# Kernel optimization log

Hardware: AMD Instinct MI355X
Metric: run time of the kernel (lower is better)

Reference implementation:

```python
import jax, jax.numpy as jnp
import numpy as np
from jax import lax

COUNTER_TARGET = 40
CONV_THRESH = 0.01


def compute_ellipticity(images):
    """images: [B,H,W] -> (e1[B], e2[B]) via iterative adaptive-Gaussian moments."""
    B, H, W = images.shape
    y = jnp.arange(H, dtype=jnp.float32) - H / 2.0 + 0.5
    x = jnp.arange(W, dtype=jnp.float32) - W / 2.0 + 0.5
    Y, X = jnp.meshgrid(y, x, indexing='ij')  # [H,W]
    X = X[None]  # [1,H,W]
    Y = Y[None]
    total = jnp.sum(images, axis=(1, 2))
    image_area = jnp.float32(H * W)

    def cond_fn(c):
        i, ax, ay, axy, mux, muy, psxx, psyy, csxx, csyy, back, e1, e2 = c
        first = jnp.equal(i, 0)
        valid = jnp.logical_not(jnp.any(jnp.isnan(csxx))) & jnp.logical_not(jnp.any(jnp.isnan(csyy)))
        converged = (jnp.max(jnp.abs(csxx - psxx)) < CONV_THRESH) & (jnp.max(jnp.abs(csyy - psyy)) < CONV_THRESH)
        converged = converged & jnp.logical_not(first)
        return (i < COUNTER_TARGET) & valid & (first | jnp.logical_not(converged))

    def body_fn(c):
        i, ax, ay, axy, mux, muy, psxx, psyy, csxx, csyy, back, e1, e2 = c
        ax = jnp.clip(ax, 0.5, 20.0)
        ay = jnp.clip(ay, 0.5, 20.0)
        axy = jnp.clip(axy, -10.0, 10.0)
        Xc = X - mux[:, None, None]
        Yc = Y - muy[:, None, None]
        alpha_denom = jnp.maximum(ax * ay, 1e-8)
        alpha_ratio = jnp.clip(axy / alpha_denom, -0.95, 0.95)
        arb_const = jnp.maximum(2.0 * (1.0 - alpha_ratio ** 2), 1e-8)
        sqrt_term = jnp.maximum(1.0 - alpha_ratio ** 2, 1e-8)
        A = 1.0 / (2.0 * jnp.pi * alpha_denom * jnp.sqrt(sqrt_term))
        A = jnp.clip(A, 1e-10, 1e10)
        ax_sq = jnp.maximum(ax ** 2, 1e-8)
        ay_sq = jnp.maximum(ay ** 2, 1e-8)
        e1t = Xc ** 2 / (arb_const * ax_sq)[:, None, None]
        e2t = Yc ** 2 / (arb_const * ay_sq)[:, None, None]
        e3t = 2.0 * axy[:, None, None] * Xc * Yc / (arb_const * ax_sq * ay_sq)[:, None, None]
        exp_term = jnp.clip(e1t + e2t - e3t, 0.0, 30.0)
        k = A[:, None, None] * jnp.exp(-exp_term)
        k = jnp.where(jnp.isnan(k), 0.0, k)
        k = jnp.where(jnp.isinf(k), 0.0, k)
        img1 = images - back[:, None, None]
        ik = img1 * k
        t1 = jnp.sum(X * Y * ik, axis=(1, 2))
        t2 = jnp.sum(ik, axis=(1, 2))
        t3 = jnp.sum(X * ik, axis=(1, 2))
        t4 = jnp.sum(Y * ik, axis=(1, 2))
        t5 = jnp.sum(X * X * ik, axis=(1, 2))
        t6 = jnp.sum(Y * Y * ik, axis=(1, 2))
        t7 = jnp.sum(k * k, axis=(1, 2))
        t2s = jnp.maximum(jnp.abs(t2), 1e-6)
        t7s = jnp.maximum(t7, 1e-6)
        flux_calc = t2 / t7s
        new_back = jnp.clip((total - flux_calc) / image_area, -1.0, 1.0)
        new_mux = jnp.clip(t3 / t2s, -W / 2.0, W / 2.0)
        new_muy = jnp.clip(t4 / t2s, -H / 2.0, H / 2.0)
        sigxx = t5 / t2s - (t3 / t2s) ** 2
        sigyy = t6 / t2s - (t4 / t2s) ** 2
        sigxy = t1 / t2s - t3 * t4 / (t2s * t2s)
        sigxx = jnp.clip(sigxx, 0.25, 100.0)
        sigyy = jnp.clip(sigyy, 0.25, 100.0)
        sigxy = jnp.clip(sigxy, -50.0, 50.0)
        nax = jnp.sqrt(jnp.clip(sigxx * 2.0, 1.0, 400.0))
        nay = jnp.sqrt(jnp.clip(sigyy * 2.0, 1.0, 400.0))
        naxy = jnp.clip(2.0 * sigxy, -20.0, 20.0)
        denom = jnp.maximum(sigxx + sigyy, 1e-6)
        ne1 = jnp.clip((sigxx - sigyy) / denom, -0.95, 0.95)
        ne2 = jnp.clip(2.0 * sigxy / denom, -0.95, 0.95)
        ne1 = jnp.where(jnp.isnan(ne1), 0.0, ne1)
        ne2 = jnp.where(jnp.isnan(ne2), 0.0, ne2)
        nax = jnp.where(jnp.isnan(nax), 2.0, nax)
        nay = jnp.where(jnp.isnan(nay), 2.0, nay)
        naxy = jnp.where(jnp.isnan(naxy), 0.0, naxy)
        return (i + 1, nax, nay, naxy, new_mux, new_muy, csxx, csyy, sigxx, sigyy, new_back, ne1, ne2)

    def step(c, _):
        cont = cond_fn(c)
        nc = body_fn(c)
        c = jax.tree_util.tree_map(lambda a, b: jnp.where(cont, b, a), c, nc)
        return c, None

    init = (jnp.int32(0),
            jnp.full([B], 2.0), jnp.full([B], 2.0), jnp.zeros([B]),
            jnp.zeros([B]), jnp.zeros([B]),
            jnp.full([B], 4.0), jnp.full([B], 4.0),
            jnp.zeros([B]), jnp.zeros([B]),
            jnp.zeros([B]), jnp.zeros([B]), jnp.zeros([B]))
    final, _ = lax.scan(step, init, None, length=COUNTER_TARGET)
    e1, e2 = final[11], final[12]
    e1 = jnp.where(jnp.isnan(e1) | jnp.isinf(e1), 0.0, e1)
    e2 = jnp.where(jnp.isnan(e2) | jnp.isinf(e2), 0.0, e2)
    return e1, e2


def blur_with_kernel(image, kernel):
    """image [B,H,W,1], kernel [B,kH,kW,1] -> per-sample SAME conv (correlation)."""
    def single(img, ker):
        ker = ker / (jnp.sum(ker) + 1e-6)
        ker = ker[..., None]  # [kH,kW,1,1] HWIO
        out = lax.conv_general_dilated(img[None], ker, window_strides=(1, 1),
                                       padding='SAME',
                                       dimension_numbers=('NHWC', 'HWIO', 'NHWC'))
        return out[0]
    return jax.vmap(single)(image, kernel)


def setup_inputs() -> dict:
    key = jax.random.key(0)
    ks = jax.random.split(key, 5)
    B, H, W, kH = 512, 96, 96, 31
    return {
        'y_pred': jax.random.uniform(ks[0], (B, H, W, 1), dtype=jnp.float32),
        'y_true': jax.random.uniform(ks[1], (B, H, W, 1), dtype=jnp.float32),
        'blurred_img': jax.random.uniform(ks[2], (B, H, W, 2), dtype=jnp.float32),
        'kernel_img': jax.random.uniform(ks[3], (B, kH, kH, 1), dtype=jnp.float32),
        'weight_map': jax.random.uniform(ks[4], (B, H, W, 1), dtype=jnp.float32),
        'current_epoch': 3,
    }


def reference(y_pred, y_true, blurred_img, kernel_img, weight_map, current_epoch):
    weighted_mse = jnp.mean(jnp.square(y_pred - y_true) * weight_map)
    sharp_true = jnp.squeeze(y_true, axis=-1)
    sharp_pred = jnp.squeeze(y_pred, axis=-1)
    e1_t, e2_t = compute_ellipticity(sharp_true)
    e1_p, e2_p = compute_ellipticity(sharp_pred)
    ellip_diff = jnp.mean((e1_t - e1_p) ** 2 + (e2_t - e2_p) ** 2)
    ellip_loss = jnp.clip(ellip_diff, 0.0, 1.0)
    ellip_weight = 0.01 + 0.1 * jnp.float32(min(current_epoch, 4))
    original_blurred = blurred_img[:, :, :, 0:1]
    reblurred = blur_with_kernel(y_pred, kernel_img)
    reblur_loss = jnp.mean(jnp.square(reblurred - original_blurred) * weight_map)
    total_loss = 100.0 * weighted_mse + 100.0 * reblur_loss + ellip_weight * ellip_loss
    return total_loss
```

## Files before the change

kernel.cpp:

```cpp
#include <hip/hip_runtime.h>

#define HW 9216
#define NBATCH 512

__device__ __forceinline__ float clampf(float v, float lo, float hi){ return fminf(fmaxf(v, lo), hi); }

__device__ __forceinline__ float waveSum(float v){
#pragma unroll
  for (int o = 32; o; o >>= 1) v += __shfl_xor(v, o, 64);
  return v;
}

__global__ __launch_bounds__(256) void mse_kernel(const float4* __restrict__ yp,
                                                  const float4* __restrict__ yt,
                                                  const float4* __restrict__ wm,
                                                  float* __restrict__ partial){
  __shared__ float red[4];
  const int tid = threadIdx.x;
  int idx = blockIdx.x * 256 + tid;
  float s = 0.f;
#pragma unroll
  for (int u = 0; u < 9; ++u){
    float4 a = yp[idx], b = yt[idx], w = wm[idx];
    float dx = a.x-b.x, dy = a.y-b.y, dz = a.z-b.z, dw = a.w-b.w;
    s += dx*dx*w.x + dy*dy*w.y + dz*dz*w.z + dw*dw*w.w;
    idx += 131072;
  }
  s = waveSum(s);
  if ((tid & 63) == 0) red[tid >> 6] = s;
  __syncthreads();
  if (tid == 0) partial[blockIdx.x] = red[0]+red[1]+red[2]+red[3];
}

__global__ __launch_bounds__(256)
void ellip_kernel(const float* __restrict__ y_true,
                  const float* __restrict__ y_pred,
                  float2* __restrict__ ebuf){
  __shared__ float wred[7][4];
  __shared__ float tred[4];
  typedef __fp16 half2_t __attribute__((ext_vector_type(2)));
  const int tid  = threadIdx.x;
  const int wave = tid >> 6, lane = tid & 63;
  const int d = blockIdx.x >> 9;
  const int b = blockIdx.x & 511;
  const int tx = tid & 31, ty = tid >> 5;

  const float* src = (d ? y_pred : y_true) + (size_t)b * HW + ty * 96 + tx;

  unsigned px2[6][3];
  float tot = 0.f;
#pragma unroll
  for (int jj = 0; jj < 6; ++jj){
#pragma unroll
    for (int c = 0; c < 3; ++c){
      float ve = src[jj*1536 + c*32];
      float vo = src[jj*1536 + 768 + c*32];
      tot += ve + vo;
      half2_t pk = __builtin_amdgcn_cvt_pkrtz(ve, vo);
      unsigned u = __builtin_bit_cast(unsigned, pk);
      asm volatile("" : "+v"(u));
      px2[jj][c] = u;
    }
  }
  tot = waveSum(tot);
  if (lane == 0) tred[wave] = tot;
  __syncthreads();
  float total;
  { float4 t = *reinterpret_cast<const float4*>(&tred[0]); total = (t.x+t.y)+(t.z+t.w); }
  __syncthreads();

  const float Ya00 = (float)ty - 47.5f;
  float Xa[3];
#pragma unroll
  for (int c = 0; c < 3; ++c){ Xa[c] = (float)(tx + 32*c) - 47.5f; }

  float zx=4.f, zy=4.f, axy=0.f, mux=0.f, muy=0.f, back=0.f, e1=0.f, e2=0.f;
  const float LOG2E = 1.4426950408889634f;
  const float NQLO  = -43.280851226668906f;

  for (int it = 0; it < 40; ++it){
    float axyc = clampf(axy, -10.f, 10.f);
    float prod = zx*zy;
    float adn  = sqrtf(prod);
    float rca  = __builtin_amdgcn_rcpf(adn);
    float ar   = clampf(axyc*rca, -0.95f, 0.95f);
    float omr  = fmaf(-ar, ar, 1.f);
    float A    = 0.15915494309189535f * rca * __builtin_amdgcn_rsqf(omr);
    float invq = __builtin_amdgcn_rcpf(2.f*omr*prod);
    float a1 = -LOG2E*zy*invq;
    float a2 = -LOG2E*zx*invq;
    float a3 = (2.f*LOG2E)*axyc*invq;
    float cX2[3], cX3[3];
#pragma unroll
    for (int c = 0; c < 3; ++c){
      float Xc = Xa[c] - mux;
      cX2[c] = a1*Xc*Xc;
      cX3[c] = a3*Xc;
    }
    float S0[3] = {0.f,0.f,0.f}, SY[3] = {0.f,0.f,0.f};
    float tYY = 0.f, tkk = 0.f;
#pragma unroll
    for (int jj = 0; jj < 6; ++jj){
      float Yae = Ya00 + 16.f*jj;
      float Yao = Yae + 8.f;
      float Yce = Yae - muy, Yco = Yao - muy;
      float he = a2*Yce*Yce, ho = a2*Yco*Yco;
      float rse = 0.f, rso = 0.f;
#pragma unroll
      for (int c = 0; c < 3; ++c){
        half2_t pk = __builtin_bit_cast(half2_t, px2[jj][c]);
        float pe = (float)pk.x, po = (float)pk.y;
        {
          float nq = fmaf(cX3[c], Yce, he + cX2[c]);
          float e  = __builtin_amdgcn_exp2f(fminf(fmaxf(nq, NQLO), 0.f));
          float ik = (pe - back)*e;
          S0[c] += ik;  SY[c] = fmaf(Yae, ik, SY[c]);  tkk = fmaf(e, e, tkk);  rse += ik;
        }
        {
          float nq = fmaf(cX3[c], Yco, ho + cX2[c]);
          float e  = __builtin_amdgcn_exp2f(fminf(fmaxf(nq, NQLO), 0.f));
          float ik = (po - back)*e;
          S0[c] += ik;  SY[c] = fmaf(Yao, ik, SY[c]);  tkk = fmaf(e, e, tkk);  rso += ik;
        }
      }
      tYY = fmaf(Yae*Yae, rse, fmaf(Yao*Yao, rso, tYY));
    }
    float tik = S0[0]+S0[1]+S0[2];
    float tX  = fmaf(Xa[2],S0[2], fmaf(Xa[1],S0[1], Xa[0]*S0[0]));
    float tXX = fmaf(Xa[2]*Xa[2],S0[2], fmaf(Xa[1]*Xa[1],S0[1], (Xa[0]*Xa[0])*S0[0]));
    float tY  = SY[0]+SY[1]+SY[2];
    float tXY = fmaf(Xa[2],SY[2], fmaf(Xa[1],SY[1], Xa[0]*SY[0]));
    tXY=waveSum(tXY); tik=waveSum(tik); tX=waveSum(tX); tY=waveSum(tY);
    tXX=waveSum(tXX); tYY=waveSum(tYY); tkk=waveSum(tkk);
    if (lane == 0){
      wred[0][wave]=tXY; wred[1][wave]=tik; wred[2][wave]=tX; wred[3][wave]=tY;
      wred[4][wave]=tXX; wred[5][wave]=tYY; wred[6][wave]=tkk;
    }
    __syncthreads();
    float T[7];
#pragma unroll
    for (int k = 0; k < 7; ++k){
      float4 r = *reinterpret_cast<const float4*>(&wred[k][0]);
      T[k] = (r.x+r.y)+(r.z+r.w);
    }
    __syncthreads();
    float T1=T[0]*A, T2=T[1]*A, T3=T[2]*A, T4=T[3]*A, T5=T[4]*A, T6=T[5]*A, T7=T[6]*A*A;
    float t2s = fmaxf(fabsf(T2), 1e-6f);
    float rt2 = __builtin_amdgcn_rcpf(t2s);
    float flux = T2 * __builtin_amdgcn_rcpf(fmaxf(T7, 1e-6f));
    back = clampf((total - flux) * (1.f/9216.f), -1.f, 1.f);
    float r3 = T3*rt2, r4 = T4*rt2;
    mux = clampf(r3, -48.f, 48.f);
    muy = clampf(r4, -48.f, 48.f);
    float sxx = clampf(T5*rt2 - r3*r3, 0.25f, 100.f);
    float syy = clampf(T6*rt2 - r4*r4, 0.25f, 100.f);
    float sxy = clampf(T1*rt2 - T3*T4*rt2*rt2, -50.f, 50.f);
    zx = clampf(sxx*2.f, 1.f, 400.f);
    zy = clampf(syy*2.f, 1.f, 400.f);
    axy = clampf(2.f*sxy, -20.f, 20.f);
    float rden = __builtin_amdgcn_rcpf(sxx+syy);
    e1 = clampf((sxx-syy)*rden, -0.95f, 0.95f);
    e2 = clampf(2.f*sxy*rden, -0.95f, 0.95f);
  }
  if (tid == 0) ebuf[d*512 + b] = make_float2(e1, e2);
}

__global__ __launch_bounds__(384, 6) void conv_kernel(const float* __restrict__ y_pred,
                                                      const float* __restrict__ kimg,
                                                      const float* __restrict__ blurred,
                                                      const float* __restrict__ wmap,
                                                      float* __restrict__ partial){
  __shared__ float P[78*128];
  __shared__ float red[6];
  const int tid = threadIdx.x;
  const int bb = blockIdx.x, b = bb >> 1, h = bb & 1;
  const int R0 = h * 48;
  const int wave = tid >> 6, lane = tid & 63;

  const float* img = y_pred + (size_t)b * HW;
  for (int u = tid; u < 78*128; u += 384){
    int pr = u >> 7, pc = u & 127;
    int ir = R0 - 15 + pr, ic = pc - 16;
    float v = 0.f;
    if ((unsigned)ir < 96u && (unsigned)ic < 96u) v = img[ir*96 + ic];
    P[u] = v;
  }
  const float* kb = kimg + (size_t)b * 961;
  float ks = 0.f;
  for (int u = tid; u < 961; u += 384) ks += kb[u];
  ks = waveSum(ks);
  if (lane == 0) red[wave] = ks;
  __syncthreads();
  const float inv = __fdividef(1.f, (red[0]+red[1]+red[2]+red[3]+red[4]+red[5]) + 1e-6f);

  const int cs = tid % 24, rq = tid / 24;
  const int c = cs*4;
  const int rr0 = R0 + rq*3;
  float acc[3][4];
#pragma unroll
  for (int q = 0; q < 3; ++q){
#pragma unroll
    for (int j = 0; j < 4; ++j) acc[q][j] = 0.f;
  }

#pragma unroll 1
  for (int s = 0; s < 33; ++s){
    float w[36];
    const float4* prow = reinterpret_cast<const float4*>(&P[(rq*3 + s)*128 + c]);
#pragma unroll
    for (int m = 0; m < 9; ++m){
      float4 v = prow[m];
      w[4*m+0]=v.x; w[4*m+1]=v.y; w[4*m+2]=v.z; w[4*m+3]=v.w;
    }
#pragma unroll
    for (int q = 0; q < 3; ++q){
      const int dy = s - q;
      if (dy >= 0 && dy <= 30){
        const float* kr = kb + dy*31;
#pragma unroll
        for (int dx = 0; dx < 31; ++dx){
          const float kv = kr[dx];
          acc[q][0] = fmaf(kv, w[dx+1], acc[q][0]);
          acc[q][1] = fmaf(kv, w[dx+2], acc[q][1]);
          acc[q][2] = fmaf(kv, w[dx+3], acc[q][2]);
          acc[q][3] = fmaf(kv, w[dx+4], acc[q][3]);
        }
      }
    }
  }

  float lsum = 0.f;
#pragma unroll
  for (int q = 0; q < 3; ++q){
#pragma unroll
    for (int j = 0; j < 4; ++j){
      const int rr = rr0+q, cc = c+j;
      const size_t pix = (size_t)b*HW + rr*96 + cc;
      float ov = acc[q][j] * inv;
      float dd = ov - blurred[2*pix];
      lsum = fmaf(dd*dd, wmap[pix], lsum);
    }
  }
  lsum = waveSum(lsum);
  __syncthreads();
  if (lane == 0) red[wave] = lsum;
  __syncthreads();
  if (tid == 0) partial[bb] = red[0]+red[1]+red[2]+red[3]+red[4]+red[5];
}

__global__ __launch_bounds__(512) void final_kernel(const float* __restrict__ msep,
                                                    const float* __restrict__ convp,
                                                    const float2* __restrict__ ebuf,
                                                    const int* __restrict__ epoch,
                                                    float* __restrict__ out){
  __shared__ float red[3][8];
  const int tid = threadIdx.x, wave = tid >> 6, lane = tid & 63;
  float a = msep[tid];
  float bsum = convp[tid] + convp[512 + tid];
  float2 et = ebuf[tid], ep = ebuf[512 + tid];
  float dx = et.x - ep.x, dy = et.y - ep.y;
  float c = dx*dx + dy*dy;
  a = waveSum(a); bsum = waveSum(bsum); c = waveSum(c);
  if (lane == 0){ red[0][wave]=a; red[1][wave]=bsum; red[2][wave]=c; }
  __syncthreads();
  if (tid == 0){
    float sa=0, sb=0, sc=0;
#pragma unroll
    for (int w = 0; w < 8; ++w){ sa+=red[0][w]; sb+=red[1][w]; sc+=red[2][w]; }
    float mse   = sa / 4718592.f;
    float rebl  = sb / 4718592.f;
    float ediff = clampf(sc / 512.f, 0.f, 1.f);
    int e = *epoch; if (e > 4) e = 4;
    float ew = 0.01f + 0.1f * (float)e;
    out[0] = 100.f*mse + 100.f*rebl + ew*ediff;
  }
}

extern "C" void kernel_launch(void* const* d_in, const int* in_sizes, int n_in,
                              void* d_out, int out_size, void* d_ws, size_t ws_size,
                              hipStream_t stream){
  const float* y_pred  = (const float*)d_in[0];
  const float* y_true  = (const float*)d_in[1];
  const float* blurred = (const float*)d_in[2];
  const float* kimg    = (const float*)d_in[3];
  const float* wmap    = (const float*)d_in[4];
  const int*   epoch   = (const int*)d_in[5];
  float* out = (float*)d_out;
  float* ws  = (float*)d_ws;

  float*  msep  = ws;
  float*  convp = ws + 512;
  float2* ebufp = (float2*)(ws + 1536);

  mse_kernel<<<512, 256, 0, stream>>>((const float4*)y_pred, (const float4*)y_true,
                                      (const float4*)wmap, msep);

  ellip_kernel<<<1024, 256, 0, stream>>>(y_true, y_pred, ebufp);

  conv_kernel<<<1024, 384, 0, stream>>>(y_pred, kimg, blurred, wmap, convp);

  final_kernel<<<1, 512, 0, stream>>>(msep, convp, ebufp, epoch, out);
}
```

Baseline: 347.2 us.

## Fuse ellipticity and convolution kernels into one interleaved launch

```diff
diff --git a/kernel.cpp b/kernel.cpp
--- a/kernel.cpp
+++ b/kernel.cpp
@@ -32,220 +32,231 @@
   if (tid == 0) partial[blockIdx.x] = red[0]+red[1]+red[2]+red[3];
 }
 
-__global__ __launch_bounds__(256)
-void ellip_kernel(const float* __restrict__ y_true,
+__global__ __launch_bounds__(384, 6)
+void fused_kernel(const float* __restrict__ y_true,
                   const float* __restrict__ y_pred,
-                  float2* __restrict__ ebuf){
-  __shared__ float wred[7][4];
-  __shared__ float tred[4];
+                  const float* __restrict__ kimg,
+                  const float* __restrict__ blurred,
+                  const float* __restrict__ wmap,
+                  float2* __restrict__ ebuf,
+                  float* __restrict__ convp){
+  extern __shared__ float smem[];
   typedef __fp16 half2_t __attribute__((ext_vector_type(2)));
-  const int tid  = threadIdx.x;
+  const int tid = threadIdx.x;
+  const int bid = blockIdx.x;
+  const int id  = bid >> 1;
   const int wave = tid >> 6, lane = tid & 63;
-  const int d = blockIdx.x >> 9;
-  const int b = blockIdx.x & 511;
-  const int tx = tid & 31, ty = tid >> 5;
-
-  const float* src = (d ? y_pred : y_true) + (size_t)b * HW + ty * 96 + tx;
-
-  unsigned px2[6][3];
-  float tot = 0.f;
-#pragma unroll
-  for (int jj = 0; jj < 6; ++jj){
-#pragma unroll
-    for (int c = 0; c < 3; ++c){
-      float ve = src[jj*1536 + c*32];
-      float vo = src[jj*1536 + 768 + c*32];
-      tot += ve + vo;
-      half2_t pk = __builtin_amdgcn_cvt_pkrtz(ve, vo);
-      unsigned u = __builtin_bit_cast(unsigned, pk);
-      asm volatile("" : "+v"(u));
-      px2[jj][c] = u;
-    }
+
+  if ((bid & 1) == 0){
+    float (*wred)[4] = (float(*)[4])smem;
+    float* tred = smem + 28;
+    if (tid < 256){
+      const int d = id >> 9;
+      const int b = id & 511;
+      const int tx = tid & 31, ty = tid >> 5;
+
+      const float* src = (d ? y_pred : y_true) + (size_t)b * HW + ty * 96 + tx;
+
+      unsigned px2[6][3];
+      float tot = 0.f;
+#pragma unroll
+      for (int jj = 0; jj < 6; ++jj){
+#pragma unroll
+        for (int c = 0; c < 3; ++c){
+          float ve = src[jj*1536 + c*32];
+          float vo = src[jj*1536 + 768 + c*32];
+          tot += ve + vo;
+          half2_t pk = __builtin_amdgcn_cvt_pkrtz(ve, vo);
+          unsigned u = __builtin_bit_cast(unsigned, pk);
+          asm volatile("" : "+v"(u));
+          px2[jj][c] = u;
+        }
+      }
+      tot = waveSum(tot);
+      if (lane == 0) tred[wave] = tot;
+      __syncthreads();
+      float total;
+      { float4 t = *reinterpret_cast<const float4*>(&tred[0]); total = (t.x+t.y)+(t.z+t.w); }
+      __syncthreads();
+
+      const float Ya00 = (float)ty - 47.5f;
+      float Xa[3];
+#pragma unroll
+      for (int c = 0; c < 3; ++c){ Xa[c] = (float)(tx + 32*c) - 47.5f; }
+
+      float zx=4.f, zy=4.f, axy=0.f, mux=0.f, muy=0.f, back=0.f, e1=0.f, e2=0.f;
+      const float LOG2E = 1.4426950408889634f;
+      const float NQLO  = -43.280851226668906f;
+
+      for (int it = 0; it < 40; ++it){
+        float axyc = clampf(axy, -10.f, 10.f);
+        float prod = zx*zy;
+        float adn  = sqrtf(prod);
+        float rca  = __builtin_amdgcn_rcpf(adn);
+        float ar   = clampf(axyc*rca, -0.95f, 0.95f);
+        float omr  = fmaf(-ar, ar, 1.f);
+        float A    = 0.15915494309189535f * rca * __builtin_amdgcn_rsqf(omr);
+        float invq = __builtin_amdgcn_rcpf(2.f*omr*prod);
+        float a1 = -LOG2E*zy*invq;
+        float a2 = -LOG2E*zx*invq;
+        float a3 = (2.f*LOG2E)*axyc*invq;
+        float cX2[3], cX3[3];
+#pragma unroll
+        for (int c = 0; c < 3; ++c){
+          float Xc = Xa[c] - mux;
+          cX2[c] = a1*Xc*Xc;
+          cX3[c] = a3*Xc;
+        }
+        float S0[3] = {0.f,0.f,0.f}, SY[3] = {0.f,0.f,0.f};
+        float tYY = 0.f, tkk = 0.f;
+#pragma unroll
+        for (int jj = 0; jj < 6; ++jj){
+          float Yae = Ya00 + 16.f*jj;
+          float Yao = Yae + 8.f;
+          float Yce = Yae - muy, Yco = Yao - muy;
+          float he = a2*Yce*Yce, ho = a2*Yco*Yco;
+          float rse = 0.f, rso = 0.f;
+#pragma unroll
+          for (int c = 0; c < 3; ++c){
+            half2_t pk = __builtin_bit_cast(half2_t, px2[jj][c]);
+            float pe = (float)pk.x, po = (float)pk.y;
+            {
+              float nq = fmaf(cX3[c], Yce, he + cX2[c]);
+              float e  = __builtin_amdgcn_exp2f(fminf(fmaxf(nq, NQLO), 0.f));
+              float ik = (pe - back)*e;
+              S0[c] += ik;  SY[c] = fmaf(Yae, ik, SY[c]);  tkk = fmaf(e, e, tkk);  rse += ik;
+            }
+            {
+              float nq = fmaf(cX3[c], Yco, ho + cX2[c]);
+              float e  = __builtin_amdgcn_exp2f(fminf(fmaxf(nq, NQLO), 0.f));
+              float ik = (po - back)*e;
+              S0[c] += ik;  SY[c] = fmaf(Yao, ik, SY[c]);  tkk = fmaf(e, e, tkk);  rso += ik;
+            }
+          }
+          tYY = fmaf(Yae*Yae, rse, fmaf(Yao*Yao, rso, tYY));
+        }
+        float tik = S0[0]+S0[1]+S0[2];
+        float tX  = fmaf(Xa[2],S0[2], fmaf(Xa[1],S0[1], Xa[0]*S0[0]));
+        float tXX = fmaf(Xa[2]*Xa[2],S0[2], fmaf(Xa[1]*Xa[1],S0[1], (Xa[0]*Xa[0])*S0[0]));
+        float tY  = SY[0]+SY[1]+SY[2];
+        float tXY = fmaf(Xa[2],SY[2], fmaf(Xa[1],SY[1], Xa[0]*SY[0]));
+        tXY=waveSum(tXY); tik=waveSum(tik); tX=waveSum(tX); tY=waveSum(tY);
+        tXX=waveSum(tXX); tYY=waveSum(tYY); tkk=waveSum(tkk);
+        if (lane == 0){
+          wred[0][wave]=tXY; wred[1][wave]=tik; wred[2][wave]=tX; wred[3][wave]=tY;
+          wred[4][wave]=tXX; wred[5][wave]=tYY; wred[6][wave]=tkk;
+        }
+        __syncthreads();
+        float T[7];
+#pragma unroll
+        for (int k = 0; k < 7; ++k){
+          float4 r = *reinterpret_cast<const float4*>(&wred[k][0]);
+          T[k] = (r.x+r.y)+(r.z+r.w);
+        }
+        __syncthreads();
+        float T1=T[0]*A, T2=T[1]*A, T3=T[2]*A, T4=T[3]*A, T5=T[4]*A, T6=T[5]*A, T7=T[6]*A*A;
+        float t2s = fmaxf(fabsf(T2), 1e-6f);
+        float rt2 = __builtin_amdgcn_rcpf(t2s);
+        float flux = T2 * __builtin_amdgcn_rcpf(fmaxf(T7, 1e-6f));
+        back = clampf((total - flux) * (1.f/9216.f), -1.f, 1.f);
+        float r3 = T3*rt2, r4 = T4*rt2;
+        mux = clampf(r3, -48.f, 48.f);
+        muy = clampf(r4, -48.f, 48.f);
+        float sxx = clampf(T5*rt2 - r3*r3, 0.25f, 100.f);
+        float syy = clampf(T6*rt2 - r4*r4, 0.25f, 100.f);
+        float sxy = clampf(T1*rt2 - T3*T4*rt2*rt2, -50.f, 50.f);
+        zx = clampf(sxx*2.f, 1.f, 400.f);
+        zy = clampf(syy*2.f, 1.f, 400.f);
+        axy = clampf(2.f*sxy, -20.f, 20.f);
+        float rden = __builtin_amdgcn_rcpf(sxx+syy);
+        e1 = clampf((sxx-syy)*rden, -0.95f, 0.95f);
+        e2 = clampf(2.f*sxy*rden, -0.95f, 0.95f);
+      }
+      if (tid == 0) ebuf[d*512 + b] = make_float2(e1, e2);
+    } else {
+      __syncthreads();
+      __syncthreads();
+      for (int it = 0; it < 40; ++it){
+        __syncthreads();
+        __syncthreads();
+      }
+    }
+  } else {
+    float* P   = smem;
+    float* red = smem + 78*128;
+    const int b = id >> 1, h = id & 1;
+    const int R0 = h * 48;
+
+    const float* img = y_pred + (size_t)b * HW;
+    for (int u = tid; u < 78*128; u += 384){
+      int pr = u >> 7, pc = u & 127;
+      int ir = R0 - 15 + pr, ic = pc - 16;
+      float v = 0.f;
+      if ((unsigned)ir < 96u && (unsigned)ic < 96u) v = img[ir*96 + ic];
+      P[u] = v;
+    }
+    const float* kb = kimg + (size_t)b * 961;
+    float ks = 0.f;
+    for (int u = tid; u < 961; u += 384) ks += kb[u];
+    ks = waveSum(ks);
+    if (lane == 0) red[wave] = ks;
+    __syncthreads();
+    const float inv = __fdividef(1.f, (red[0]+red[1]+red[2]+red[3]+red[4]+red[5]) + 1e-6f);
+
+    const int cs = tid % 24, rq = tid / 24;
+    const int c = cs*4;
+    const int rr0 = R0 + rq*3;
+    float acc[3][4];
+#pragma unroll
+    for (int q = 0; q < 3; ++q){
+#pragma unroll
+      for (int j = 0; j < 4; ++j) acc[q][j] = 0.f;
+    }
+
+#pragma unroll 1
+    for (int s = 0; s < 33; ++s){
+      float w[36];
+      const float4* prow = reinterpret_cast<const float4*>(&P[(rq*3 + s)*128 + c]);
+#pragma unroll
+      for (int m = 0; m < 9; ++m){
+        float4 v = prow[m];
+        w[4*m+0]=v.x; w[4*m+1]=v.y; w[4*m+2]=v.z; w[4*m+3]=v.w;
+      }
+#pragma unroll
+      for (int q = 0; q < 3; ++q){
+        const int dy = s - q;
+        if (dy >= 0 && dy <= 30){
+          const float* kr = kb + dy*31;
+#pragma unroll
+          for (int dx = 0; dx < 31; ++dx){
+            const float kv = kr[dx];
+            acc[q][0] = fmaf(kv, w[dx+1], acc[q][0]);
+            acc[q][1] = fmaf(kv, w[dx+2], acc[q][1]);
+            acc[q][2] = fmaf(kv, w[dx+3], acc[q][2]);
+            acc[q][3] = fmaf(kv, w[dx+4], acc[q][3]);
+          }
+        }
+      }
+    }
+
+    float lsum = 0.f;
+#pragma unroll
+    for (int q = 0; q < 3; ++q){
+#pragma unroll
+      for (int j = 0; j < 4; ++j){
+        const int rr = rr0+q, cc = c+j;
+        const size_t pix = (size_t)b*HW + rr*96 + cc;
+        float ov = acc[q][j] * inv;
+        float dd = ov - blurred[2*pix];
+        lsum = fmaf(dd*dd, wmap[pix], lsum);
+      }
+    }
+    lsum = waveSum(lsum);
+    __syncthreads();
+    if (lane == 0) red[wave] = lsum;
+    __syncthreads();
+    if (tid == 0) convp[id] = red[0]+red[1]+red[2]+red[3]+red[4]+red[5];
   }
-  tot = waveSum(tot);
-  if (lane == 0) tred[wave] = tot;
-  __syncthreads();
-  float total;
-  { float4 t = *reinterpret_cast<const float4*>(&tred[0]); total = (t.x+t.y)+(t.z+t.w); }
-  __syncthreads();
-
-  const float Ya00 = (float)ty - 47.5f;
-  float Xa[3];
-#pragma unroll
-  for (int c = 0; c < 3; ++c){ Xa[c] = (float)(tx + 32*c) - 47.5f; }
-
-  float zx=4.f, zy=4.f, axy=0.f, mux=0.f, muy=0.f, back=0.f, e1=0.f, e2=0.f;
-  const float LOG2E = 1.4426950408889634f;
-  const float NQLO  = -43.280851226668906f;
-
-  for (int it = 0; it < 40; ++it){
-    float axyc = clampf(axy, -10.f, 10.f);
-    float prod = zx*zy;
-    float adn  = sqrtf(prod);
-    float rca  = __builtin_amdgcn_rcpf(adn);
-    float ar   = clampf(axyc*rca, -0.95f, 0.95f);
-    float omr  = fmaf(-ar, ar, 1.f);
-    float A    = 0.15915494309189535f * rca * __builtin_amdgcn_rsqf(omr);
-    float invq = __builtin_amdgcn_rcpf(2.f*omr*prod);
-    float a1 = -LOG2E*zy*invq;
-    float a2 = -LOG2E*zx*invq;
-    float a3 = (2.f*LOG2E)*axyc*invq;
-    float cX2[3], cX3[3];
-#pragma unroll
-    for (int c = 0; c < 3; ++c){
-      float Xc = Xa[c] - mux;
-      cX2[c] = a1*Xc*Xc;
-      cX3[c] = a3*Xc;
-    }
-    float S0[3] = {0.f,0.f,0.f}, SY[3] = {0.f,0.f,0.f};
-    float tYY = 0.f, tkk = 0.f;
-#pragma unroll
-    for (int jj = 0; jj < 6; ++jj){
-      float Yae = Ya00 + 16.f*jj;
-      float Yao = Yae + 8.f;
-      float Yce = Yae - muy, Yco = Yao - muy;
-      float he = a2*Yce*Yce, ho = a2*Yco*Yco;
-      float rse = 0.f, rso = 0.f;
-#pragma unroll
-      for (int c = 0; c < 3; ++c){
-        half2_t pk = __builtin_bit_cast(half2_t, px2[jj][c]);
-        float pe = (float)pk.x, po = (float)pk.y;
-        {
-          float nq = fmaf(cX3[c], Yce, he + cX2[c]);
-          float e  = __builtin_amdgcn_exp2f(fminf(fmaxf(nq, NQLO), 0.f));
-          float ik = (pe - back)*e;
-          S0[c] += ik;  SY[c] = fmaf(Yae, ik, SY[c]);  tkk = fmaf(e, e, tkk);  rse += ik;
-        }
-        {
-          float nq = fmaf(cX3[c], Yco, ho + cX2[c]);
-          float e  = __builtin_amdgcn_exp2f(fminf(fmaxf(nq, NQLO), 0.f));
-          float ik = (po - back)*e;
-          S0[c] += ik;  SY[c] = fmaf(Yao, ik, SY[c]);  tkk = fmaf(e, e, tkk);  rso += ik;
-        }
-      }
-      tYY = fmaf(Yae*Yae, rse, fmaf(Yao*Yao, rso, tYY));
-    }
-    float tik = S0[0]+S0[1]+S0[2];
-    float tX  = fmaf(Xa[2],S0[2], fmaf(Xa[1],S0[1], Xa[0]*S0[0]));
-    float tXX = fmaf(Xa[2]*Xa[2],S0[2], fmaf(Xa[1]*Xa[1],S0[1], (Xa[0]*Xa[0])*S0[0]));
-    float tY  = SY[0]+SY[1]+SY[2];
-    float tXY = fmaf(Xa[2],SY[2], fmaf(Xa[1],SY[1], Xa[0]*SY[0]));
-    tXY=waveSum(tXY); tik=waveSum(tik); tX=waveSum(tX); tY=waveSum(tY);
-    tXX=waveSum(tXX); tYY=waveSum(tYY); tkk=waveSum(tkk);
-    if (lane == 0){
-      wred[0][wave]=tXY; wred[1][wave]=tik; wred[2][wave]=tX; wred[3][wave]=tY;
-      wred[4][wave]=tXX; wred[5][wave]=tYY; wred[6][wave]=tkk;
-    }
-    __syncthreads();
-    float T[7];
-#pragma unroll
-    for (int k = 0; k < 7; ++k){
-      float4 r = *reinterpret_cast<const float4*>(&wred[k][0]);
-      T[k] = (r.x+r.y)+(r.z+r.w);
-    }
-    __syncthreads();
-    float T1=T[0]*A, T2=T[1]*A, T3=T[2]*A, T4=T[3]*A, T5=T[4]*A, T6=T[5]*A, T7=T[6]*A*A;
-    float t2s = fmaxf(fabsf(T2), 1e-6f);
-    float rt2 = __builtin_amdgcn_rcpf(t2s);
-    float flux = T2 * __builtin_amdgcn_rcpf(fmaxf(T7, 1e-6f));
-    back = clampf((total - flux) * (1.f/9216.f), -1.f, 1.f);
-    float r3 = T3*rt2, r4 = T4*rt2;
-    mux = clampf(r3, -48.f, 48.f);
-    muy = clampf(r4, -48.f, 48.f);
-    float sxx = clampf(T5*rt2 - r3*r3, 0.25f, 100.f);
-    float syy = clampf(T6*rt2 - r4*r4, 0.25f, 100.f);
-    float sxy = clampf(T1*rt2 - T3*T4*rt2*rt2, -50.f, 50.f);
-    zx = clampf(sxx*2.f, 1.f, 400.f);
-    zy = clampf(syy*2.f, 1.f, 400.f);
-    axy = clampf(2.f*sxy, -20.f, 20.f);
-    float rden = __builtin_amdgcn_rcpf(sxx+syy);
-    e1 = clampf((sxx-syy)*rden, -0.95f, 0.95f);
-    e2 = clampf(2.f*sxy*rden, -0.95f, 0.95f);
-  }
-  if (tid == 0) ebuf[d*512 + b] = make_float2(e1, e2);
-}
-
-__global__ __launch_bounds__(384, 6) void conv_kernel(const float* __restrict__ y_pred,
-                                                      const float* __restrict__ kimg,
-                                                      const float* __restrict__ blurred,
-                                                      const float* __restrict__ wmap,
-                                                      float* __restrict__ partial){
-  __shared__ float P[78*128];
-  __shared__ float red[6];
-  const int tid = threadIdx.x;
-  const int bb = blockIdx.x, b = bb >> 1, h = bb & 1;
-  const int R0 = h * 48;
-  const int wave = tid >> 6, lane = tid & 63;
-
-  const float* img = y_pred + (size_t)b * HW;
-  for (int u = tid; u < 78*128; u += 384){
-    int pr = u >> 7, pc = u & 127;
-    int ir = R0 - 15 + pr, ic = pc - 16;
-    float v = 0.f;
-    if ((unsigned)ir < 96u && (unsigned)ic < 96u) v = img[ir*96 + ic];
-    P[u] = v;
-  }
-  const float* kb = kimg + (size_t)b * 961;
-  float ks = 0.f;
-  for (int u = tid; u < 961; u += 384) ks += kb[u];
-  ks = waveSum(ks);
-  if (lane == 0) red[wave] = ks;
-  __syncthreads();
-  const float inv = __fdividef(1.f, (red[0]+red[1]+red[2]+red[3]+red[4]+red[5]) + 1e-6f);
-
-  const int cs = tid % 24, rq = tid / 24;
-  const int c = cs*4;
-  const int rr0 = R0 + rq*3;
-  float acc[3][4];
-#pragma unroll
-  for (int q = 0; q < 3; ++q){
-#pragma unroll
-    for (int j = 0; j < 4; ++j) acc[q][j] = 0.f;
-  }
-
-#pragma unroll 1
-  for (int s = 0; s < 33; ++s){
-    float w[36];
-    const float4* prow = reinterpret_cast<const float4*>(&P[(rq*3 + s)*128 + c]);
-#pragma unroll
-    for (int m = 0; m < 9; ++m){
-      float4 v = prow[m];
-      w[4*m+0]=v.x; w[4*m+1]=v.y; w[4*m+2]=v.z; w[4*m+3]=v.w;
-    }
-#pragma unroll
-    for (int q = 0; q < 3; ++q){
-      const int dy = s - q;
-      if (dy >= 0 && dy <= 30){
-        const float* kr = kb + dy*31;
-#pragma unroll
-        for (int dx = 0; dx < 31; ++dx){
-          const float kv = kr[dx];
-          acc[q][0] = fmaf(kv, w[dx+1], acc[q][0]);
-          acc[q][1] = fmaf(kv, w[dx+2], acc[q][1]);
-          acc[q][2] = fmaf(kv, w[dx+3], acc[q][2]);
-          acc[q][3] = fmaf(kv, w[dx+4], acc[q][3]);
-        }
-      }
-    }
-  }
-
-  float lsum = 0.f;
-#pragma unroll
-  for (int q = 0; q < 3; ++q){
-#pragma unroll
-    for (int j = 0; j < 4; ++j){
-      const int rr = rr0+q, cc = c+j;
-      const size_t pix = (size_t)b*HW + rr*96 + cc;
-      float ov = acc[q][j] * inv;
-      float dd = ov - blurred[2*pix];
-      lsum = fmaf(dd*dd, wmap[pix], lsum);
-    }
-  }
-  lsum = waveSum(lsum);
-  __syncthreads();
-  if (lane == 0) red[wave] = lsum;
-  __syncthreads();
-  if (tid == 0) partial[bb] = red[0]+red[1]+red[2]+red[3]+red[4]+red[5];
 }
 
 __global__ __launch_bounds__(512) void final_kernel(const float* __restrict__ msep,
@@ -295,9 +306,8 @@
   mse_kernel<<<512, 256, 0, stream>>>((const float4*)y_pred, (const float4*)y_true,
                                       (const float4*)wmap, msep);
 
-  ellip_kernel<<<1024, 256, 0, stream>>>(y_true, y_pred, ebufp);
-
-  conv_kernel<<<1024, 384, 0, stream>>>(y_pred, kimg, blurred, wmap, convp);
+  fused_kernel<<<2048, 384, 39960, stream>>>(y_true, y_pred, kimg, blurred, wmap,
+                                             ebufp, convp);
 
   final_kernel<<<1, 512, 0, stream>>>(msep, convp, ebufp, epoch, out);
 }
```

Measured after the change: 453.3 us. 1.31x slower.
